# Kernel tuning notes

Measured on AMD Instinct MI355X. Metric: run time of the kernel, lower is better.

The kernel has to match this reference:

```python
import jax, jax.numpy as jnp
import numpy as np

B, S, H = 2, 2048, 1024
NH, KVH, HD = 16, 4, 64
EPS = 1e-6


def setup_inputs() -> dict:
    key = jax.random.key(0)
    ks = jax.random.split(key, 6)
    hidden_states = jax.random.normal(ks[0], (B, S, H), jnp.float32)
    # additive causal mask [B,1,S,S]
    neg = jnp.finfo(jnp.float32).min
    causal = jnp.where(jnp.tril(jnp.ones((S, S), bool)), 0.0, neg)
    attention_mask = jnp.broadcast_to(causal[None, None], (B, 1, S, S))
    # RoPE cos/sin [B,S,HD]
    pos = jnp.arange(S, dtype=jnp.float32)
    inv_freq = 1.0 / (10000.0 ** (jnp.arange(0, HD, 2, dtype=jnp.float32) / HD))
    freqs = pos[:, None] * inv_freq[None, :]          # [S, HD//2]
    emb = jnp.concatenate([freqs, freqs], axis=-1)    # [S, HD]
    cos = jnp.broadcast_to(jnp.cos(emb)[None], (B, S, HD))
    sin = jnp.broadcast_to(jnp.sin(emb)[None], (B, S, HD))
    scale = 0.02
    q_weight = jax.random.normal(ks[1], (NH * HD, H), jnp.float32) * scale
    k_weight = jax.random.normal(ks[2], (KVH * HD, H), jnp.float32) * scale
    v_weight = jax.random.normal(ks[3], (KVH * HD, H), jnp.float32) * scale
    o_weight = jax.random.normal(ks[4], (H, NH * HD), jnp.float32) * scale
    q_norm_weight = jnp.ones((HD,), jnp.float32)
    k_norm_weight = jnp.ones((HD,), jnp.float32)
    return dict(hidden_states=hidden_states, attention_mask=attention_mask,
                cos=cos, sin=sin, q_weight=q_weight, k_weight=k_weight,
                v_weight=v_weight, o_weight=o_weight,
                q_norm_weight=q_norm_weight, k_norm_weight=k_norm_weight)


def _rotate_half(x):
    x1, x2 = x[..., : x.shape[-1] // 2], x[..., x.shape[-1] // 2:]
    return jnp.concatenate([-x2, x1], axis=-1)


def _rms_norm(x, w, eps=EPS):
    xf = x.astype(jnp.float32)
    var = jnp.mean(xf * xf, axis=-1, keepdims=True)
    return (w * (xf * jax.lax.rsqrt(var + eps)).astype(x.dtype))


def reference(hidden_states, attention_mask, cos, sin, q_weight, k_weight,
              v_weight, o_weight, q_norm_weight, k_norm_weight):
    b, s, h = hidden_states.shape
    # projections (torch F.linear: x @ W.T)
    q = (hidden_states @ q_weight.T).reshape(b, s, NH, HD).transpose(0, 2, 1, 3)
    k = (hidden_states @ k_weight.T).reshape(b, s, KVH, HD).transpose(0, 2, 1, 3)
    v = (hidden_states @ v_weight.T).reshape(b, s, KVH, HD).transpose(0, 2, 1, 3)
    # per-head QK RMSNorm (Qwen3 style)
    q = _rms_norm(q, q_norm_weight)
    k = _rms_norm(k, k_norm_weight)
    # RoPE, cos/sin broadcast over head axis
    c, si = cos[:, None], sin[:, None]                 # [B,1,S,HD]
    q = q * c + _rotate_half(q) * si
    k = k * c + _rotate_half(k) * si
    # GQA: repeat kv heads
    rep = NH // KVH
    k = jnp.repeat(k, rep, axis=1)
    v = jnp.repeat(v, rep, axis=1)
    # attention
    scores = jnp.einsum('bhqd,bhkd->bhqk', q, k) * (HD ** -0.5)
    scores = scores + attention_mask[:, :, :, :s]
    attn = jax.nn.softmax(scores.astype(jnp.float32), axis=-1).astype(q.dtype)
    out = jnp.einsum('bhqk,bhkd->bhqd', attn, v)
    out = out.transpose(0, 2, 1, 3).reshape(b, s, NH * HD)
    return out @ o_weight.T
```

## Files before the change

### kernel.cpp

```cpp
#include <hip/hip_runtime.h>

typedef unsigned short u16;
typedef __attribute__((ext_vector_type(4))) float f32x4;
typedef __attribute__((ext_vector_type(8))) __bf16 bf16x8;
typedef __attribute__((ext_vector_type(8))) unsigned short u16x8;
typedef __attribute__((ext_vector_type(4))) unsigned short u16x4;

#define NEGINF -3.0e38f

#define BB 2
#define SS 2048
#define HH 1024
#define NHEAD 16
#define KVHEAD 4
#define HD 64
#define BS (BB*SS)
#define NQKV 1536

#define QSCALE 0.18033688f
#define SMBIAS -11.5415603f

__device__ __forceinline__ u16 f2bf(float f) {
  union { float f; unsigned int u; } v; v.f = f;
  unsigned int r = v.u + 0x7FFFu + ((v.u >> 16) & 1u);
  return (u16)(r >> 16);
}
__device__ __forceinline__ float bf2f(u16 h) {
  union { unsigned int u; float f; } v; v.u = ((unsigned int)h) << 16;
  return v.f;
}

typedef const unsigned int __attribute__((address_space(1)))* gp_t;
typedef unsigned int __attribute__((address_space(3)))* lp_t;
__device__ __forceinline__ void gload_lds16(const void* g, void* l) {
  __builtin_amdgcn_global_load_lds((gp_t)g, (lp_t)l, 16, 0, 0);
}

__global__ __launch_bounds__(256) void cvt_all(
    const float* __restrict__ h, const float* __restrict__ qw,
    const float* __restrict__ kw, const float* __restrict__ vw,
    const float* __restrict__ ow,
    u16* __restrict__ Xb, u16* __restrict__ Wqkv, u16* __restrict__ Wo) {
  long i = ((long)blockIdx.x * 256 + threadIdx.x) * 4;
  const float* src; u16* dst;
  if (i < 4194304L)      { src = h  + i;             dst = Xb   + i; }
  else if (i < 5242880L) { src = qw + (i - 4194304); dst = Wqkv + (i - 4194304); }
  else if (i < 5505024L) { src = kw + (i - 5242880); dst = Wqkv + (i - 4194304); }
  else if (i < 5767168L) { src = vw + (i - 5505024); dst = Wqkv + (i - 4194304); }
  else                   { src = ow + (i - 5767168); dst = Wo   + (i - 5767168); }
  float4 v = *(const float4*)src;
  u16x4 o;
  o.x = f2bf(v.x); o.y = f2bf(v.y); o.z = f2bf(v.z); o.w = f2bf(v.w);
  *(u16x4*)dst = o;
}

template<int EPI>
__global__ __launch_bounds__(256) void gemm_bt(
    const u16* __restrict__ A, const u16* __restrict__ Bw,
    float* __restrict__ Cf,
    u16* __restrict__ Qb, u16* __restrict__ Kb, u16* __restrict__ Vb,
    const float* __restrict__ cosb, const float* __restrict__ sinb,
    const float* __restrict__ qnw, const float* __restrict__ knw,
    int M, int N, int K)
{
  __shared__ u16 As[2][64 * 64];
  __shared__ u16 Bs[2][128 * 64];
  const int tid = threadIdx.x;
  const int w = tid >> 6, l = tid & 63;
  const int lg = l >> 4, lc = l & 15;
  const int m0 = blockIdx.y * 64, n0 = blockIdx.x * 128;
  const int wr = (w >> 1) * 32, wc = (w & 1) * 64;

  const f32x4 vzero = {0.f, 0.f, 0.f, 0.f};
  f32x4 acc[2][4];
#pragma unroll
  for (int i = 0; i < 2; ++i)
#pragma unroll
    for (int j = 0; j < 4; ++j) acc[i][j] = vzero;

  const u16* Ap = A + (size_t)m0 * K;
  const u16* Bp = Bw + (size_t)n0 * K;
  const int nk = K >> 6;

  const int arow = tid >> 3, ach = tid & 7;

#define GSTAGE(bufi, kt)                                                         \
  {                                                                              \
    _Pragma("unroll") for (int c = 0; c < 2; ++c) {                              \
      int row = c * 32 + arow;                                                   \
      gload_lds16(Ap + (size_t)row * K + (kt) * 64 + (ach ^ (row & 7)) * 8,      \
                  (char*)As[bufi] + c * 4096 + w * 1024);                        \
    }                                                                            \
    _Pragma("unroll") for (int c = 0; c < 4; ++c) {                              \
      int row = c * 32 + arow;                                                   \
      gload_lds16(Bp + (size_t)row * K + (kt) * 64 + (ach ^ (row & 7)) * 8,      \
                  (char*)Bs[bufi] + c * 4096 + w * 1024);                        \
    }                                                                            \
  }

  GSTAGE(0, 0)
  __syncthreads();

  for (int kt = 0; kt < nk; ++kt) {
    const int cur = kt & 1;
    if (kt + 1 < nk) GSTAGE(cur ^ 1, kt + 1)

    bf16x8 af[2][2], bfr[4][2];
#pragma unroll
    for (int i = 0; i < 2; ++i) {
      int row = wr + i * 16 + lc;
#pragma unroll
      for (int c = 0; c < 2; ++c)
        af[i][c] = *(const bf16x8*)&As[cur][row * 64 + (((c * 4 + lg) ^ (lc & 7)) << 3)];
    }
#pragma unroll
    for (int i = 0; i < 4; ++i) {
      int row = wc + i * 16 + lc;
#pragma unroll
      for (int c = 0; c < 2; ++c)
        bfr[i][c] = *(const bf16x8*)&Bs[cur][row * 64 + (((c * 4 + lg) ^ (lc & 7)) << 3)];
    }
    __builtin_amdgcn_s_setprio(1);
#pragma unroll
    for (int c = 0; c < 2; ++c)
#pragma unroll
      for (int am = 0; am < 2; ++am)
#pragma unroll
        for (int bn = 0; bn < 4; ++bn)
          acc[am][bn] = __builtin_amdgcn_mfma_f32_16x16x32_bf16(af[am][c], bfr[bn][c], acc[am][bn], 0, 0, 0);
    __builtin_amdgcn_s_setprio(0);

    if (kt + 1 < nk) __syncthreads();
  }
#undef GSTAGE

  if (EPI == 1) {
#pragma unroll
    for (int am = 0; am < 2; ++am)
#pragma unroll
      for (int bn = 0; bn < 4; ++bn)
#pragma unroll
        for (int r = 0; r < 4; ++r) {
          int m = m0 + wr + am * 16 + lg * 4 + r;
          int n = n0 + wc + bn * 16 + lc;
          Cf[(size_t)m * N + n] = acc[am][bn][r];
        }
  } else {
    const int nb = n0 + wc;
    if (nb < 1280) {
      const bool isQ = (nb < 1024);
      const int head = isQ ? (nb >> 6) : ((nb - 1024) >> 6);
      u16* dst = isQ ? (Qb + ((size_t)head * SS) * HD)
                     : (Kb + ((size_t)head * SS) * HD);
      const size_t hstride = (size_t)(isQ ? NHEAD : KVHEAD) * SS * HD;
      const float* wt = isQ ? qnw : knw;
      const float posc = isQ ? QSCALE : 1.0f;
      float wt4[4];
#pragma unroll
      for (int bn = 0; bn < 4; ++bn) wt4[bn] = wt[bn * 16 + lc];
#pragma unroll
      for (int am = 0; am < 2; ++am)
#pragma unroll
        for (int r = 0; r < 4; ++r) {
          int m = m0 + wr + am * 16 + lg * 4 + r;
          int bb = m >> 11, s2 = m & 2047;
          float ss = 0.f;
#pragma unroll
          for (int bn = 0; bn < 4; ++bn) ss += acc[am][bn][r] * acc[am][bn][r];
          ss += __shfl_xor(ss, 1);
          ss += __shfl_xor(ss, 2);
          ss += __shfl_xor(ss, 4);
          ss += __shfl_xor(ss, 8);
          float rs = rsqrtf(ss * (1.0f / 64.0f) + 1e-6f);
          size_t cbase = ((size_t)bb * SS + s2) * HD;
          size_t obase = bb * hstride + (size_t)s2 * HD;
#pragma unroll
          for (int bn = 0; bn < 4; ++bn) {
            int d = bn * 16 + lc;
            float xn = acc[am][bn][r] * rs * wt4[bn];
            float xp = acc[am][bn ^ 2][r] * rs * wt4[bn ^ 2];
            float rot = (bn < 2) ? -xp : xp;
            float o = (xn * cosb[cbase + d] + rot * sinb[cbase + d]) * posc;
            dst[obase + d] = f2bf(o);
          }
        }
    } else {
      const int kh = (nb - 1280) >> 6;
#pragma unroll
      for (int am = 0; am < 2; ++am)
#pragma unroll
        for (int r = 0; r < 4; ++r) {
          int m = m0 + wr + am * 16 + lg * 4 + r;
          int bb = m >> 11, s2 = m & 2047;
#pragma unroll
          for (int bn = 0; bn < 4; ++bn) {
            int d = bn * 16 + lc;
            Vb[(((size_t)bb * KVHEAD + kh) * HD + d) * SS + s2] = f2bf(acc[am][bn][r]);
          }
        }
    }
  }
}

__global__ __launch_bounds__(256) void attn_kernel(
    const u16* __restrict__ Qb, const u16* __restrict__ Kb,
    const u16* __restrict__ Vt, u16* __restrict__ Ob)
{
  __shared__ u16 Ks[3][64 * 64];
  __shared__ u16 Vs[3][64 * 64];

  const int tid = threadIdx.x;
  const int w = tid >> 6, l = tid & 63;
  const int lg = l >> 4, lc = l & 15;

  const int bid = blockIdx.x;
  const int a = bid & 7, hb = (bid >> 3) & 31, hi = bid >> 8;
  const int qt = hi ? (15 - a) : a;
  const int h = hb & 15, b = hb >> 4;
  const int q0 = qt * 128;
  const int kvh = h >> 2;

  const u16* Qp = Qb + (((size_t)b * NHEAD + h) * SS + q0 + w * 32) * HD;
  const u16* Kp = Kb + ((size_t)b * KVHEAD + kvh) * SS * HD;
  const u16* Vp = Vt + ((size_t)b * KVHEAD + kvh) * (size_t)HD * SS;

  bf16x8 qa[2][2];
#pragma unroll
  for (int qf = 0; qf < 2; ++qf)
#pragma unroll
    for (int c = 0; c < 2; ++c)
      qa[qf][c] = *(const bf16x8*)(Qp + (qf * 16 + lc) * HD + c * 32 + lg * 8);

  const f32x4 vzero = {0.f, 0.f, 0.f, 0.f};
  const f32x4 zbias = {SMBIAS, SMBIAS, SMBIAS, SMBIAS};
  f32x4 acc[2][4];
  float lsum[2] = {0.f, 0.f};
#pragma unroll
  for (int qf = 0; qf < 2; ++qf)
#pragma unroll
    for (int df = 0; df < 4; ++df) acc[qf][df] = vzero;

  const int srow0 = w * 8 + (l >> 3);
  const int srow1 = srow0 + 32;
  const int sswz = (l >> 3) ^ ((w & 1) << 2);
  const int ss0 = (l & 7) ^ sswz;
  const int nt = 2 * qt + 2;

  int ko[8], vo[8];
#pragma unroll
  for (int f = 0; f < 4; ++f) {
    int row = ((lc >> 2) << 3) + ((f & 1) << 2) + (lc & 3) + ((f >> 1) << 5);
    int swz = (((f & 1) << 2) + (lc & 3)) ^ (((lc >> 2) & 1) << 2);
    ko[2 * f]     = row * 64 + ((lg ^ swz) << 3);
    ko[2 * f + 1] = row * 64 + (((4 + lg) ^ swz) << 3);
  }
#pragma unroll
  for (int df = 0; df < 4; ++df) {
    int vrow = 16 * df + lc;
    int vswz = (lc & 7) ^ (((lc >> 3) & 1) << 2);
    vo[2 * df]     = vrow * 64 + ((lg ^ vswz) << 3);
    vo[2 * df + 1] = vrow * 64 + (((4 + lg) ^ vswz) << 3);
  }

#define STAGE(bufi, kvbase)                                                          \
  gload_lds16(Kp + (size_t)((kvbase) + srow0) * HD + ss0 * 8, (char*)Ks[bufi] + w * 1024);        \
  gload_lds16(Kp + (size_t)((kvbase) + srow1) * HD + ss0 * 8, (char*)Ks[bufi] + 4096 + w * 1024); \
  gload_lds16(Vp + (size_t)srow0 * SS + (kvbase) + ss0 * 8, (char*)Vs[bufi] + w * 1024);          \
  gload_lds16(Vp + (size_t)srow1 * SS + (kvbase) + ss0 * 8, (char*)Vs[bufi] + 4096 + w * 1024);

  STAGE(0, 0)
  STAGE(1, 64)
  __syncthreads();

  int rd = 0;
  for (int kt = 0; kt < nt; ++kt) {
    int st = rd + 2; if (st >= 3) st -= 3;
    if (kt + 2 < nt) { STAGE(st, (kt + 2) * 64) }

    const int kv0 = kt * 64;
    if (kv0 <= q0 + w * 32 + 31) {
      const u16* KsB = Ks[rd];
      const u16* VsB = Vs[rd];

      bf16x8 kb[8], vb[8];
#pragma unroll
      for (int i = 0; i < 8; ++i) kb[i] = *(const bf16x8*)&KsB[ko[i]];
#pragma unroll
      for (int i = 0; i < 8; ++i) vb[i] = *(const bf16x8*)&VsB[vo[i]];

      const bool diag = (kv0 + 63 > q0 + w * 32);
      bf16x8 pa[2][2];
#pragma unroll
      for (int c = 0; c < 2; ++c) {
        f32x4 sv[2][2];
#pragma unroll
        for (int fs = 0; fs < 2; ++fs) {
          const int f = 2 * c + fs;
#pragma unroll
          for (int qf = 0; qf < 2; ++qf) {
            f32x4 z = zbias;
            z = __builtin_amdgcn_mfma_f32_16x16x32_bf16(kb[2 * f], qa[qf][0], z, 0, 0, 0);
            z = __builtin_amdgcn_mfma_f32_16x16x32_bf16(kb[2 * f + 1], qa[qf][1], z, 0, 0, 0);
            sv[qf][fs] = z;
          }
        }
        if (diag) {
          const int keyb = kv0 + c * 32 + lg * 8;
#pragma unroll
          for (int qf = 0; qf < 2; ++qf) {
            const int qi = q0 + w * 32 + qf * 16 + lc;
#pragma unroll
            for (int fs = 0; fs < 2; ++fs)
#pragma unroll
              for (int rr = 0; rr < 4; ++rr) {
                int key = keyb + fs * 4 + rr;
                if (key > qi) sv[qf][fs][rr] = NEGINF;
              }
          }
        }
#pragma unroll
        for (int qf = 0; qf < 2; ++qf) {
#pragma unroll
          for (int fs = 0; fs < 2; ++fs)
#pragma unroll
            for (int rr = 0; rr < 4; ++rr) {
              float p = __builtin_amdgcn_exp2f(sv[qf][fs][rr]);
              sv[qf][fs][rr] = p;
              lsum[qf] += p;
            }
#pragma unroll
          for (int j = 0; j < 8; ++j)
            pa[qf][c][j] = (__bf16)sv[qf][j >> 2][j & 3];
        }
      }

#pragma unroll
      for (int df = 0; df < 4; ++df)
#pragma unroll
        for (int qf = 0; qf < 2; ++qf) {
          acc[qf][df] = __builtin_amdgcn_mfma_f32_16x16x32_bf16(pa[qf][0], vb[2 * df], acc[qf][df], 0, 0, 0);
          acc[qf][df] = __builtin_amdgcn_mfma_f32_16x16x32_bf16(pa[qf][1], vb[2 * df + 1], acc[qf][df], 0, 0, 0);
        }
    }

    if (kt + 1 < nt) __syncthreads();
    rd = (rd + 1 == 3) ? 0 : rd + 1;
  }
#undef STAGE

#pragma unroll
  for (int qf = 0; qf < 2; ++qf) {
    float t = lsum[qf];
    t += __shfl_xor(t, 16);
    t += __shfl_xor(t, 32);
#pragma unroll
    for (int r = 0; r < 4; ++r) {
      float dnm = __shfl(t, lg * 4 + r);
      float inv = 1.0f / dnm;
      int qi = q0 + w * 32 + qf * 16 + lg * 4 + r;
#pragma unroll
      for (int df = 0; df < 4; ++df)
        Ob[((size_t)b * SS + qi) * (NHEAD * HD) + h * HD + df * 16 + lc] =
            f2bf(acc[qf][df][r] * inv);
    }
  }
}

extern "C" void kernel_launch(void* const* d_in, const int* in_sizes, int n_in,
                              void* d_out, int out_size, void* d_ws, size_t ws_size,
                              hipStream_t stream) {
  const float* hidden = (const float*)d_in[0];
  const float* cosb = (const float*)d_in[2];
  const float* sinb = (const float*)d_in[3];
  const float* qw = (const float*)d_in[4];
  const float* kw = (const float*)d_in[5];
  const float* vw = (const float*)d_in[6];
  const float* ow = (const float*)d_in[7];
  const float* qnw = (const float*)d_in[8];
  const float* knw = (const float*)d_in[9];
  float* out = (float*)d_out;

  u16* Xb   = (u16*)d_ws;
  u16* Wqkv = Xb + (size_t)BS * HH;
  u16* Wo   = Wqkv + (size_t)NQKV * HH;
  u16* Qb   = Wo + (size_t)HH * HH;
  u16* Kb   = Qb + (size_t)BB * NHEAD * SS * HD;
  u16* Vb   = Kb + (size_t)BB * KVHEAD * SS * HD;
  u16* Ab   = Vb + (size_t)BB * KVHEAD * SS * HD;

  cvt_all<<<6656, 256, 0, stream>>>(hidden, qw, kw, vw, ow, Xb, Wqkv, Wo);

  gemm_bt<0><<<dim3(NQKV / 128, BS / 64), 256, 0, stream>>>(
      Xb, Wqkv, nullptr, Qb, Kb, Vb, cosb, sinb, qnw, knw, BS, NQKV, HH);

  attn_kernel<<<512, 256, 0, stream>>>(Qb, Kb, Vb, Ab);

  gemm_bt<1><<<dim3(HH / 128, BS / 64), 256, 0, stream>>>(
      Ab, Wo, out, nullptr, nullptr, nullptr, nullptr, nullptr, nullptr, nullptr, BS, HH, HH);
}
```

Measured before the change: 90.49 us.

## Software-pipeline the QK^T MFMAs for the next KV tile behind the current softmax and PV

The attention loop now computes the QK^T scores for tile kt+1 while it runs the exp2 softmax and the PV MFMAs for tile kt. The goal is to overlap matrix-core work with the vector exp work and the LDS reads. K and V fragments are now loaded from LDS per fragment rather than all at once. The per-wave skip of fully masked tiles is gone, so waves near the diagonal do redundant masked work. Carrying two score tiles also raises register pressure.

```diff
diff --git a/kernel.cpp b/kernel.cpp
--- a/kernel.cpp
+++ b/kernel.cpp
@@ -268,85 +268,96 @@
   gload_lds16(Vp + (size_t)srow0 * SS + (kvbase) + ss0 * 8, (char*)Vs[bufi] + w * 1024);          \
   gload_lds16(Vp + (size_t)srow1 * SS + (kvbase) + ss0 * 8, (char*)Vs[bufi] + 4096 + w * 1024);
 
+#define QK_TILE(dstsv, bufi)                                                         \
+  {                                                                                  \
+    const u16* KsB_ = Ks[bufi];                                                      \
+    _Pragma("unroll") for (int f_ = 0; f_ < 4; ++f_) {                               \
+      bf16x8 k0_ = *(const bf16x8*)&KsB_[ko[2 * f_]];                                \
+      bf16x8 k1_ = *(const bf16x8*)&KsB_[ko[2 * f_ + 1]];                            \
+      _Pragma("unroll") for (int qf_ = 0; qf_ < 2; ++qf_) {                          \
+        f32x4 z_ = zbias;                                                            \
+        z_ = __builtin_amdgcn_mfma_f32_16x16x32_bf16(k0_, qa[qf_][0], z_, 0, 0, 0);  \
+        z_ = __builtin_amdgcn_mfma_f32_16x16x32_bf16(k1_, qa[qf_][1], z_, 0, 0, 0);  \
+        dstsv[qf_][f_] = z_;                                                         \
+      }                                                                              \
+    }                                                                                \
+  }
+
   STAGE(0, 0)
   STAGE(1, 64)
   __syncthreads();
+
+  f32x4 svc[2][4];
+  QK_TILE(svc, 0)
 
   int rd = 0;
   for (int kt = 0; kt < nt; ++kt) {
     int st = rd + 2; if (st >= 3) st -= 3;
     if (kt + 2 < nt) { STAGE(st, (kt + 2) * 64) }
 
+    f32x4 svn[2][4];
+    int rn = rd + 1; if (rn >= 3) rn -= 3;
+    if (kt + 1 < nt) { QK_TILE(svn, rn) }
+
     const int kv0 = kt * 64;
-    if (kv0 <= q0 + w * 32 + 31) {
-      const u16* KsB = Ks[rd];
+    if (kv0 + 63 > q0 + w * 32) {
+#pragma unroll
+      for (int qf = 0; qf < 2; ++qf) {
+        const int qi = q0 + w * 32 + qf * 16 + lc;
+#pragma unroll
+        for (int f = 0; f < 4; ++f)
+#pragma unroll
+          for (int rr = 0; rr < 4; ++rr) {
+            int key = kv0 + ((f >> 1) << 5) + ((f & 1) << 2) + lg * 8 + rr;
+            if (key > qi) svc[qf][f][rr] = NEGINF;
+          }
+      }
+    }
+
+    bf16x8 pa[2][2];
+#pragma unroll
+    for (int qf = 0; qf < 2; ++qf) {
+#pragma unroll
+      for (int f = 0; f < 4; ++f)
+#pragma unroll
+        for (int rr = 0; rr < 4; ++rr) {
+          float p = __builtin_amdgcn_exp2f(svc[qf][f][rr]);
+          svc[qf][f][rr] = p;
+          lsum[qf] += p;
+        }
+#pragma unroll
+      for (int c = 0; c < 2; ++c)
+#pragma unroll
+        for (int j = 0; j < 8; ++j)
+          pa[qf][c][j] = (__bf16)svc[qf][2 * c + (j >> 2)][j & 3];
+    }
+
+    {
       const u16* VsB = Vs[rd];
-
-      bf16x8 kb[8], vb[8];
-#pragma unroll
-      for (int i = 0; i < 8; ++i) kb[i] = *(const bf16x8*)&KsB[ko[i]];
-#pragma unroll
-      for (int i = 0; i < 8; ++i) vb[i] = *(const bf16x8*)&VsB[vo[i]];
-
-      const bool diag = (kv0 + 63 > q0 + w * 32);
-      bf16x8 pa[2][2];
-#pragma unroll
-      for (int c = 0; c < 2; ++c) {
-        f32x4 sv[2][2];
-#pragma unroll
-        for (int fs = 0; fs < 2; ++fs) {
-          const int f = 2 * c + fs;
-#pragma unroll
-          for (int qf = 0; qf < 2; ++qf) {
-            f32x4 z = zbias;
-            z = __builtin_amdgcn_mfma_f32_16x16x32_bf16(kb[2 * f], qa[qf][0], z, 0, 0, 0);
-            z = __builtin_amdgcn_mfma_f32_16x16x32_bf16(kb[2 * f + 1], qa[qf][1], z, 0, 0, 0);
-            sv[qf][fs] = z;
-          }
-        }
-        if (diag) {
-          const int keyb = kv0 + c * 32 + lg * 8;
-#pragma unroll
-          for (int qf = 0; qf < 2; ++qf) {
-            const int qi = q0 + w * 32 + qf * 16 + lc;
-#pragma unroll
-            for (int fs = 0; fs < 2; ++fs)
-#pragma unroll
-              for (int rr = 0; rr < 4; ++rr) {
-                int key = keyb + fs * 4 + rr;
-                if (key > qi) sv[qf][fs][rr] = NEGINF;
-              }
-          }
-        }
+#pragma unroll
+      for (int df = 0; df < 4; ++df) {
+        bf16x8 v0 = *(const bf16x8*)&VsB[vo[2 * df]];
+        bf16x8 v1 = *(const bf16x8*)&VsB[vo[2 * df + 1]];
 #pragma unroll
         for (int qf = 0; qf < 2; ++qf) {
-#pragma unroll
-          for (int fs = 0; fs < 2; ++fs)
-#pragma unroll
-            for (int rr = 0; rr < 4; ++rr) {
-              float p = __builtin_amdgcn_exp2f(sv[qf][fs][rr]);
-              sv[qf][fs][rr] = p;
-              lsum[qf] += p;
-            }
-#pragma unroll
-          for (int j = 0; j < 8; ++j)
-            pa[qf][c][j] = (__bf16)sv[qf][j >> 2][j & 3];
+          acc[qf][df] = __builtin_amdgcn_mfma_f32_16x16x32_bf16(pa[qf][0], v0, acc[qf][df], 0, 0, 0);
+          acc[qf][df] = __builtin_amdgcn_mfma_f32_16x16x32_bf16(pa[qf][1], v1, acc[qf][df], 0, 0, 0);
         }
       }
-
-#pragma unroll
-      for (int df = 0; df < 4; ++df)
-#pragma unroll
-        for (int qf = 0; qf < 2; ++qf) {
-          acc[qf][df] = __builtin_amdgcn_mfma_f32_16x16x32_bf16(pa[qf][0], vb[2 * df], acc[qf][df], 0, 0, 0);
-          acc[qf][df] = __builtin_amdgcn_mfma_f32_16x16x32_bf16(pa[qf][1], vb[2 * df + 1], acc[qf][df], 0, 0, 0);
-        }
-    }
-
-    if (kt + 1 < nt) __syncthreads();
+    }
+
+    if (kt + 1 < nt) {
+      __syncthreads();
+#pragma unroll
+      for (int qf = 0; qf < 2; ++qf)
+#pragma unroll
+        for (int f = 0; f < 4; ++f)
+          svc[qf][f] = svn[qf][f];
+    }
     rd = (rd + 1 == 3) ? 0 : rd + 1;
   }
 #undef STAGE
+#undef QK_TILE
 
 #pragma unroll
   for (int qf = 0; qf < 2; ++qf) {
```

Measured after the change: 94.27 us. 4.2% more time.

## Restructure attention into single-wave blocks with per-wave double buffering

Applied to the files above, without the earlier changes.

The attention kernel changes from 256-thread blocks handling 128 query rows each to 64-thread single-wavefront blocks handling 32 query rows, launched as 2048 blocks. Block ids are remapped so that neighbouring blocks share a KV head and heavy and light causal tiles are interleaved. Each wave stages its own K/V tiles into a double buffer with vmcnt waits instead of a triple buffer plus __syncthreads, and masking is applied only on the last tile. s_setprio is raised around the MFMA phases, and the design accepts more redundant K/V loading across blocks in exchange for dropping block-wide barriers and balancing load better.

```diff
diff --git a/kernel.cpp b/kernel.cpp
--- a/kernel.cpp
+++ b/kernel.cpp
@@ -202,25 +202,27 @@
   }
 }
 
-__global__ __launch_bounds__(256) void attn_kernel(
+__global__ __launch_bounds__(64, 2) void attn_kernel(
     const u16* __restrict__ Qb, const u16* __restrict__ Kb,
     const u16* __restrict__ Vt, u16* __restrict__ Ob)
 {
-  __shared__ u16 Ks[3][64 * 64];
-  __shared__ u16 Vs[3][64 * 64];
-
-  const int tid = threadIdx.x;
-  const int w = tid >> 6, l = tid & 63;
+  __shared__ u16 Ks[2][64 * 64];
+  __shared__ u16 Vs[2][64 * 64];
+
+  const int l = threadIdx.x;
   const int lg = l >> 4, lc = l & 15;
 
   const int bid = blockIdx.x;
-  const int a = bid & 7, hb = (bid >> 3) & 31, hi = bid >> 8;
-  const int qt = hi ? (15 - a) : a;
-  const int h = hb & 15, b = hb >> 4;
-  const int q0 = qt * 128;
-  const int kvh = h >> 2;
-
-  const u16* Qp = Qb + (((size_t)b * NHEAD + h) * SS + q0 + w * 32) * HD;
+  const int bkvh = bid & 7, b = bkvh >> 2, kvh = bkvh & 3;
+  const int s = (bid >> 3) & 31, hq = s & 3, v = s >> 2;
+  const int r = bid >> 8;
+  const int m = (r >> 1) * 8 + v;
+  const int jt = (r & 1) ? m : 63 - m;
+  const int h = kvh * 4 + hq;
+  const int q0 = jt * 32;
+  const int nt = (jt >> 1) + 1;
+
+  const u16* Qp = Qb + (((size_t)b * NHEAD + h) * SS + q0) * HD;
   const u16* Kp = Kb + ((size_t)b * KVHEAD + kvh) * SS * HD;
   const u16* Vp = Vt + ((size_t)b * KVHEAD + kvh) * (size_t)HD * SS;
 
@@ -240,11 +242,15 @@
 #pragma unroll
     for (int df = 0; df < 4; ++df) acc[qf][df] = vzero;
 
-  const int srow0 = w * 8 + (l >> 3);
-  const int srow1 = srow0 + 32;
-  const int sswz = (l >> 3) ^ ((w & 1) << 2);
-  const int ss0 = (l & 7) ^ sswz;
-  const int nt = 2 * qt + 2;
+  const int lrow = l >> 3;
+  const int sb = (l & 7) ^ lrow;
+  int koffs[8], voffs[8];
+#pragma unroll
+  for (int i = 0; i < 8; ++i) {
+    int sl = (sb ^ ((i & 1) << 2)) * 8;
+    koffs[i] = (8 * i + lrow) * HD + sl;
+    voffs[i] = (8 * i + lrow) * SS + sl;
+  }
 
   int ko[8], vo[8];
 #pragma unroll
@@ -262,89 +268,91 @@
     vo[2 * df + 1] = vrow * 64 + (((4 + lg) ^ vswz) << 3);
   }
 
-#define STAGE(bufi, kvbase)                                                          \
-  gload_lds16(Kp + (size_t)((kvbase) + srow0) * HD + ss0 * 8, (char*)Ks[bufi] + w * 1024);        \
-  gload_lds16(Kp + (size_t)((kvbase) + srow1) * HD + ss0 * 8, (char*)Ks[bufi] + 4096 + w * 1024); \
-  gload_lds16(Vp + (size_t)srow0 * SS + (kvbase) + ss0 * 8, (char*)Vs[bufi] + w * 1024);          \
-  gload_lds16(Vp + (size_t)srow1 * SS + (kvbase) + ss0 * 8, (char*)Vs[bufi] + 4096 + w * 1024);
+#define STAGE(bufi, kv0_)                                                        \
+  {                                                                              \
+    _Pragma("unroll") for (int i_ = 0; i_ < 8; ++i_) {                           \
+      gload_lds16(Kp + (size_t)(kv0_)*HD + koffs[i_], (char*)Ks[bufi] + i_ * 1024); \
+      gload_lds16(Vp + (kv0_) + voffs[i_], (char*)Vs[bufi] + i_ * 1024);         \
+    }                                                                            \
+  }
 
   STAGE(0, 0)
-  STAGE(1, 64)
-  __syncthreads();
-
-  int rd = 0;
-  for (int kt = 0; kt < nt; ++kt) {
-    int st = rd + 2; if (st >= 3) st -= 3;
-    if (kt + 2 < nt) { STAGE(st, (kt + 2) * 64) }
-
-    const int kv0 = kt * 64;
-    if (kv0 <= q0 + w * 32 + 31) {
-      const u16* KsB = Ks[rd];
-      const u16* VsB = Vs[rd];
-
-      bf16x8 kb[8], vb[8];
-#pragma unroll
-      for (int i = 0; i < 8; ++i) kb[i] = *(const bf16x8*)&KsB[ko[i]];
-#pragma unroll
-      for (int i = 0; i < 8; ++i) vb[i] = *(const bf16x8*)&VsB[vo[i]];
-
-      const bool diag = (kv0 + 63 > q0 + w * 32);
-      bf16x8 pa[2][2];
-#pragma unroll
-      for (int c = 0; c < 2; ++c) {
-        f32x4 sv[2][2];
-#pragma unroll
-        for (int fs = 0; fs < 2; ++fs) {
-          const int f = 2 * c + fs;
-#pragma unroll
-          for (int qf = 0; qf < 2; ++qf) {
-            f32x4 z = zbias;
-            z = __builtin_amdgcn_mfma_f32_16x16x32_bf16(kb[2 * f], qa[qf][0], z, 0, 0, 0);
-            z = __builtin_amdgcn_mfma_f32_16x16x32_bf16(kb[2 * f + 1], qa[qf][1], z, 0, 0, 0);
-            sv[qf][fs] = z;
+
+  for (int t = 0; t < nt; ++t) {
+    const int cur = t & 1;
+    if (t + 1 < nt) {
+      STAGE(cur ^ 1, (t + 1) * 64)
+      asm volatile("s_waitcnt vmcnt(16)" ::: "memory");
+    } else {
+      asm volatile("s_waitcnt vmcnt(0)" ::: "memory");
+    }
+    __builtin_amdgcn_sched_barrier(0);
+
+    const u16* KsB = Ks[cur];
+    const u16* VsB = Vs[cur];
+
+    bf16x8 kb[8];
+#pragma unroll
+    for (int i = 0; i < 8; ++i) kb[i] = *(const bf16x8*)&KsB[ko[i]];
+    f32x4 sv[2][4];
+    __builtin_amdgcn_s_setprio(1);
+#pragma unroll
+    for (int f = 0; f < 4; ++f)
+#pragma unroll
+      for (int qf = 0; qf < 2; ++qf) {
+        f32x4 z = zbias;
+        z = __builtin_amdgcn_mfma_f32_16x16x32_bf16(kb[2 * f], qa[qf][0], z, 0, 0, 0);
+        z = __builtin_amdgcn_mfma_f32_16x16x32_bf16(kb[2 * f + 1], qa[qf][1], z, 0, 0, 0);
+        sv[qf][f] = z;
+      }
+    __builtin_amdgcn_s_setprio(0);
+
+    bf16x8 vb[8];
+#pragma unroll
+    for (int i = 0; i < 8; ++i) vb[i] = *(const bf16x8*)&VsB[vo[i]];
+
+    if (t == nt - 1) {
+      const int keyb = t * 64 + lg * 8;
+#pragma unroll
+      for (int qf = 0; qf < 2; ++qf) {
+        const int qi = q0 + qf * 16 + lc;
+#pragma unroll
+        for (int f = 0; f < 4; ++f)
+#pragma unroll
+          for (int rr = 0; rr < 4; ++rr) {
+            int key = keyb + ((f >> 1) << 5) + ((f & 1) << 2) + rr;
+            if (key > qi) sv[qf][f][rr] = NEGINF;
           }
+      }
+    }
+
+    bf16x8 pa[2][2];
+#pragma unroll
+    for (int qf = 0; qf < 2; ++qf) {
+#pragma unroll
+      for (int f = 0; f < 4; ++f)
+#pragma unroll
+        for (int rr = 0; rr < 4; ++rr) {
+          float p = __builtin_amdgcn_exp2f(sv[qf][f][rr]);
+          sv[qf][f][rr] = p;
+          lsum[qf] += p;
         }
-        if (diag) {
-          const int keyb = kv0 + c * 32 + lg * 8;
-#pragma unroll
-          for (int qf = 0; qf < 2; ++qf) {
-            const int qi = q0 + w * 32 + qf * 16 + lc;
-#pragma unroll
-            for (int fs = 0; fs < 2; ++fs)
-#pragma unroll
-              for (int rr = 0; rr < 4; ++rr) {
-                int key = keyb + fs * 4 + rr;
-                if (key > qi) sv[qf][fs][rr] = NEGINF;
-              }
-          }
-        }
-#pragma unroll
-        for (int qf = 0; qf < 2; ++qf) {
-#pragma unroll
-          for (int fs = 0; fs < 2; ++fs)
-#pragma unroll
-            for (int rr = 0; rr < 4; ++rr) {
-              float p = __builtin_amdgcn_exp2f(sv[qf][fs][rr]);
-              sv[qf][fs][rr] = p;
-              lsum[qf] += p;
-            }
-#pragma unroll
-          for (int j = 0; j < 8; ++j)
-            pa[qf][c][j] = (__bf16)sv[qf][j >> 2][j & 3];
-        }
+#pragma unroll
+      for (int c = 0; c < 2; ++c)
+#pragma unroll
+        for (int j = 0; j < 8; ++j)
+          pa[qf][c][j] = (__bf16)sv[qf][2 * c + (j >> 2)][j & 3];
+    }
+
+    __builtin_amdgcn_s_setprio(1);
+#pragma unroll
+    for (int df = 0; df < 4; ++df)
+#pragma unroll
+      for (int qf = 0; qf < 2; ++qf) {
+        acc[qf][df] = __builtin_amdgcn_mfma_f32_16x16x32_bf16(pa[qf][0], vb[2 * df], acc[qf][df], 0, 0, 0);
+        acc[qf][df] = __builtin_amdgcn_mfma_f32_16x16x32_bf16(pa[qf][1], vb[2 * df + 1], acc[qf][df], 0, 0, 0);
       }
-
-#pragma unroll
-      for (int df = 0; df < 4; ++df)
-#pragma unroll
-        for (int qf = 0; qf < 2; ++qf) {
-          acc[qf][df] = __builtin_amdgcn_mfma_f32_16x16x32_bf16(pa[qf][0], vb[2 * df], acc[qf][df], 0, 0, 0);
-          acc[qf][df] = __builtin_amdgcn_mfma_f32_16x16x32_bf16(pa[qf][1], vb[2 * df + 1], acc[qf][df], 0, 0, 0);
-        }
-    }
-
-    if (kt + 1 < nt) __syncthreads();
-    rd = (rd + 1 == 3) ? 0 : rd + 1;
+    __builtin_amdgcn_s_setprio(0);
   }
 #undef STAGE
 
@@ -354,14 +362,14 @@
     t += __shfl_xor(t, 16);
     t += __shfl_xor(t, 32);
 #pragma unroll
-    for (int r = 0; r < 4; ++r) {
-      float dnm = __shfl(t, lg * 4 + r);
+    for (int rr = 0; rr < 4; ++rr) {
+      float dnm = __shfl(t, lg * 4 + rr);
       float inv = 1.0f / dnm;
-      int qi = q0 + w * 32 + qf * 16 + lg * 4 + r;
+      int qi = q0 + qf * 16 + lg * 4 + rr;
 #pragma unroll
       for (int df = 0; df < 4; ++df)
         Ob[((size_t)b * SS + qi) * (NHEAD * HD) + h * HD + df * 16 + lc] =
-            f2bf(acc[qf][df][r] * inv);
+            f2bf(acc[qf][df][rr] * inv);
     }
   }
 }
@@ -393,7 +401,7 @@
   gemm_bt<0><<<dim3(NQKV / 128, BS / 64), 256, 0, stream>>>(
       Xb, Wqkv, nullptr, Qb, Kb, Vb, cosb, sinb, qnw, knw, BS, NQKV, HH);
 
-  attn_kernel<<<512, 256, 0, stream>>>(Qb, Kb, Vb, Ab);
+  attn_kernel<<<2048, 64, 0, stream>>>(Qb, Kb, Vb, Ab);
 
   gemm_bt<1><<<dim3(HH / 128, BS / 64), 256, 0, stream>>>(
       Ab, Wo, out, nullptr, nullptr, nullptr, nullptr, nullptr, nullptr, nullptr, BS, HH, HH);
```

Result: slower. 97.62 us (+7.9%).

## Restructure attention KV loop to 128-key double-buffered tiles with per-chunk causal skip

Applied to the files above, without the earlier changes.

The attention kernel now stages 128-key K/V tiles into two LDS buffers instead of 64-key tiles in a triple buffer, which halves the number of loop iterations and block-wide barriers. Each tile is processed in four 32-key chunks. Causal skipping is decided per chunk, and K/V fragments are loaded from LDS just before use rather than all up front. s_setprio is raised around the MFMA sections to favour matrix issue. The cost is a larger LDS footprint per block, which may reduce occupancy, and only one tile of prefetch lookahead.

```diff
diff --git a/kernel.cpp b/kernel.cpp
--- a/kernel.cpp
+++ b/kernel.cpp
@@ -206,8 +206,8 @@
     const u16* __restrict__ Qb, const u16* __restrict__ Kb,
     const u16* __restrict__ Vt, u16* __restrict__ Ob)
 {
-  __shared__ u16 Ks[3][64 * 64];
-  __shared__ u16 Vs[3][64 * 64];
+  __shared__ u16 Ks[2][128 * 64];
+  __shared__ u16 Vs[2][64 * 128];
 
   const int tid = threadIdx.x;
   const int w = tid >> 6, l = tid & 63;
@@ -240,72 +240,73 @@
 #pragma unroll
     for (int df = 0; df < 4; ++df) acc[qf][df] = vzero;
 
-  const int srow0 = w * 8 + (l >> 3);
-  const int srow1 = srow0 + 32;
-  const int sswz = (l >> 3) ^ ((w & 1) << 2);
-  const int ss0 = (l & 7) ^ sswz;
-  const int nt = 2 * qt + 2;
-
-  int ko[8], vo[8];
-#pragma unroll
-  for (int f = 0; f < 4; ++f) {
-    int row = ((lc >> 2) << 3) + ((f & 1) << 2) + (lc & 3) + ((f >> 1) << 5);
-    int swz = (((f & 1) << 2) + (lc & 3)) ^ (((lc >> 2) & 1) << 2);
-    ko[2 * f]     = row * 64 + ((lg ^ swz) << 3);
-    ko[2 * f + 1] = row * 64 + (((4 + lg) ^ swz) << 3);
-  }
-#pragma unroll
-  for (int df = 0; df < 4; ++df) {
-    int vrow = 16 * df + lc;
-    int vswz = (lc & 7) ^ (((lc >> 3) & 1) << 2);
-    vo[2 * df]     = vrow * 64 + ((lg ^ vswz) << 3);
-    vo[2 * df + 1] = vrow * 64 + (((4 + lg) ^ vswz) << 3);
-  }
-
-#define STAGE(bufi, kvbase)                                                          \
-  gload_lds16(Kp + (size_t)((kvbase) + srow0) * HD + ss0 * 8, (char*)Ks[bufi] + w * 1024);        \
-  gload_lds16(Kp + (size_t)((kvbase) + srow1) * HD + ss0 * 8, (char*)Ks[bufi] + 4096 + w * 1024); \
-  gload_lds16(Vp + (size_t)srow0 * SS + (kvbase) + ss0 * 8, (char*)Vs[bufi] + w * 1024);          \
-  gload_lds16(Vp + (size_t)srow1 * SS + (kvbase) + ss0 * 8, (char*)Vs[bufi] + 4096 + w * 1024);
+  const int krow_s = tid >> 3;
+  const int kslot = (tid & 7) ^ (krow_s & 7) ^ (((krow_s >> 3) & 1) << 2);
+  const int vrow_s = tid >> 4;
+  const int vslot = (tid & 15) ^ (vrow_s & 7) ^ (((vrow_s >> 3) & 1) << 2);
+  const int nt = qt + 1;
+
+  int kob[2][2];
+#pragma unroll
+  for (int fs = 0; fs < 2; ++fs) {
+    int rb = ((lc >> 2) << 3) + (fs << 2) + (lc & 3);
+    int swz = ((fs << 2) + (lc & 3)) ^ (((lc >> 2) & 1) << 2);
+    kob[fs][0] = rb * 64 + ((lg ^ swz) << 3);
+    kob[fs][1] = rb * 64 + (((4 + lg) ^ swz) << 3);
+  }
+  const int vswz = (lc & 7) ^ (((lc >> 3) & 1) << 2);
+  int vrowoff[4], vsl[4];
+#pragma unroll
+  for (int df = 0; df < 4; ++df) vrowoff[df] = (16 * df + lc) * 128;
+#pragma unroll
+  for (int c = 0; c < 4; ++c) vsl[c] = (((c * 4 + lg) ^ vswz) << 3);
+
+#define STAGE(bufi, kv0_)                                                            \
+  {                                                                                  \
+    _Pragma("unroll") for (int i_ = 0; i_ < 4; ++i_) {                               \
+      gload_lds16(Kp + (size_t)((kv0_) + i_ * 32 + krow_s) * HD + kslot * 8,         \
+                  (char*)Ks[bufi] + i_ * 4096 + w * 1024);                           \
+      gload_lds16(Vp + (size_t)(i_ * 16 + vrow_s) * SS + (kv0_) + vslot * 8,         \
+                  (char*)Vs[bufi] + i_ * 4096 + w * 1024);                           \
+    }                                                                                \
+  }
 
   STAGE(0, 0)
-  STAGE(1, 64)
   __syncthreads();
 
-  int rd = 0;
-  for (int kt = 0; kt < nt; ++kt) {
-    int st = rd + 2; if (st >= 3) st -= 3;
-    if (kt + 2 < nt) { STAGE(st, (kt + 2) * 64) }
-
-    const int kv0 = kt * 64;
-    if (kv0 <= q0 + w * 32 + 31) {
-      const u16* KsB = Ks[rd];
-      const u16* VsB = Vs[rd];
-
-      bf16x8 kb[8], vb[8];
-#pragma unroll
-      for (int i = 0; i < 8; ++i) kb[i] = *(const bf16x8*)&KsB[ko[i]];
-#pragma unroll
-      for (int i = 0; i < 8; ++i) vb[i] = *(const bf16x8*)&VsB[vo[i]];
-
-      const bool diag = (kv0 + 63 > q0 + w * 32);
-      bf16x8 pa[2][2];
-#pragma unroll
-      for (int c = 0; c < 2; ++c) {
+  for (int t = 0; t < nt; ++t) {
+    const int cur = t & 1;
+    if (t + 1 < nt) STAGE(cur ^ 1, (t + 1) * 128)
+
+    const int kv0 = t * 128;
+    const u16* KsB = Ks[cur];
+    const u16* VsB = Vs[cur];
+
+#pragma unroll
+    for (int c = 0; c < 4; ++c) {
+      const int kb0 = kv0 + c * 32;
+      if (kb0 <= q0 + w * 32 + 31) {
+        bf16x8 kf[2][2];
+#pragma unroll
+        for (int fs = 0; fs < 2; ++fs)
+#pragma unroll
+          for (int hh = 0; hh < 2; ++hh)
+            kf[fs][hh] = *(const bf16x8*)&KsB[kob[fs][hh] + c * 2048];
+
         f32x4 sv[2][2];
-#pragma unroll
-        for (int fs = 0; fs < 2; ++fs) {
-          const int f = 2 * c + fs;
+        __builtin_amdgcn_s_setprio(1);
+#pragma unroll
+        for (int fs = 0; fs < 2; ++fs)
 #pragma unroll
           for (int qf = 0; qf < 2; ++qf) {
             f32x4 z = zbias;
-            z = __builtin_amdgcn_mfma_f32_16x16x32_bf16(kb[2 * f], qa[qf][0], z, 0, 0, 0);
-            z = __builtin_amdgcn_mfma_f32_16x16x32_bf16(kb[2 * f + 1], qa[qf][1], z, 0, 0, 0);
+            z = __builtin_amdgcn_mfma_f32_16x16x32_bf16(kf[fs][0], qa[qf][0], z, 0, 0, 0);
+            z = __builtin_amdgcn_mfma_f32_16x16x32_bf16(kf[fs][1], qa[qf][1], z, 0, 0, 0);
             sv[qf][fs] = z;
           }
-        }
-        if (diag) {
-          const int keyb = kv0 + c * 32 + lg * 8;
+        __builtin_amdgcn_s_setprio(0);
+
+        if (kb0 + 31 > q0 + w * 32) {
 #pragma unroll
           for (int qf = 0; qf < 2; ++qf) {
             const int qi = q0 + w * 32 + qf * 16 + lc;
@@ -313,11 +314,13 @@
             for (int fs = 0; fs < 2; ++fs)
 #pragma unroll
               for (int rr = 0; rr < 4; ++rr) {
-                int key = keyb + fs * 4 + rr;
+                int key = kb0 + fs * 4 + lg * 8 + rr;
                 if (key > qi) sv[qf][fs][rr] = NEGINF;
               }
           }
         }
+
+        bf16x8 pa[2];
 #pragma unroll
         for (int qf = 0; qf < 2; ++qf) {
 #pragma unroll
@@ -330,21 +333,22 @@
             }
 #pragma unroll
           for (int j = 0; j < 8; ++j)
-            pa[qf][c][j] = (__bf16)sv[qf][j >> 2][j & 3];
-        }
+            pa[qf][j] = (__bf16)sv[qf][j >> 2][j & 3];
+        }
+
+        __builtin_amdgcn_s_setprio(1);
+#pragma unroll
+        for (int df = 0; df < 4; ++df) {
+          bf16x8 vb = *(const bf16x8*)&VsB[vrowoff[df] + vsl[c]];
+#pragma unroll
+          for (int qf = 0; qf < 2; ++qf)
+            acc[qf][df] = __builtin_amdgcn_mfma_f32_16x16x32_bf16(pa[qf], vb, acc[qf][df], 0, 0, 0);
+        }
+        __builtin_amdgcn_s_setprio(0);
       }
-
-#pragma unroll
-      for (int df = 0; df < 4; ++df)
-#pragma unroll
-        for (int qf = 0; qf < 2; ++qf) {
-          acc[qf][df] = __builtin_amdgcn_mfma_f32_16x16x32_bf16(pa[qf][0], vb[2 * df], acc[qf][df], 0, 0, 0);
-          acc[qf][df] = __builtin_amdgcn_mfma_f32_16x16x32_bf16(pa[qf][1], vb[2 * df + 1], acc[qf][df], 0, 0, 0);
-        }
     }
 
-    if (kt + 1 < nt) __syncthreads();
-    rd = (rd + 1 == 3) ? 0 : rd + 1;
+    if (t + 1 < nt) __syncthreads();
   }
 #undef STAGE
 
```

Result: no change. 90.34 us (-0.2%).
